# Performance work log

Hardware: AMD Instinct MI355X
Metric: run time of the kernel (lower is better)

Reference implementation:

```python
import jax, jax.numpy as jnp
import numpy as np

B, N, F_IN = 2048, 64, 49   # batch of molecules, max atoms, atom feature size
D, H, L = 256, 8, 6         # conv_dim, num_heads, n_GAT_layer
DK = D // H                 # per-head dim
FC = 128                    # fc_dim
ALPHA = 0.2                 # LeakyReLU slope in GAT
NEG_INF = -1e9


def setup_inputs() -> dict:
    key = jax.random.key(0)
    ks = jax.random.split(key, 10)
    # --- padded molecular graphs ---
    n_atoms = jax.random.randint(ks[0], (B,), 16, N + 1)
    valid = jnp.arange(N)[None, :] < n_atoms[:, None]                  # [B,N]
    r = jax.random.uniform(ks[1], (B, N, N))
    adj = ((r + jnp.swapaxes(r, 1, 2)) * 0.5) < 0.08                   # symmetric sparse bonds
    adj = adj | jnp.eye(N, dtype=bool)[None]                           # self loops
    adj = adj & valid[:, :, None] & valid[:, None, :]                  # zero padded atoms
    A = adj.astype(jnp.float32)                                        # [B,N,N]
    x = jax.random.normal(ks[2], (B, N, F_IN), dtype=jnp.float32)      # [B,N,49]
    # --- parameters (xavier-like scaling) ---
    W_emb = jax.random.normal(ks[3], (D, F_IN), dtype=jnp.float32) * 0.08
    gat_W = jax.random.normal(ks[4], (L, D, D), dtype=jnp.float32) * 0.06
    gat_b = jnp.zeros((L, D), dtype=jnp.float32)
    gat_a = jax.random.normal(ks[5], (L, H, 2 * DK), dtype=jnp.float32) * 0.1
    fc_W1 = jax.random.normal(ks[6], (FC, D), dtype=jnp.float32) * 0.07
    fc_b1 = jnp.zeros((FC,), dtype=jnp.float32)
    fc_W2 = jax.random.normal(ks[7], (FC, FC), dtype=jnp.float32) * 0.09
    fc_b2 = jnp.zeros((FC,), dtype=jnp.float32)
    fc_W3 = jax.random.normal(ks[8], (1, FC), dtype=jnp.float32) * 0.09
    fc_b3 = jnp.zeros((1,), dtype=jnp.float32)
    return dict(x=x, A=A, W_emb=W_emb, gat_W=gat_W, gat_b=gat_b, gat_a=gat_a,
                fc_W1=fc_W1, fc_b1=fc_b1, fc_W2=fc_W2, fc_b2=fc_b2,
                fc_W3=fc_W3, fc_b3=fc_b3)


def _gat_layer(x, A, W, b, a):
    # x: [B,N,D], A: [B,N,N], W: [D,D], b: [D], a: [H,2*DK]
    Bm, Nn, Dd = x.shape
    h = (x @ W.T + b).reshape(Bm, Nn, H, DK)                           # [B,N,H,DK]
    a_src, a_dst = a[:, :DK], a[:, DK:]                                # [H,DK]
    e_src = jnp.einsum('bnhd,hd->bnh', h, a_src)                       # [B,N,H]
    e_dst = jnp.einsum('bnhd,hd->bnh', h, a_dst)
    e = jax.nn.leaky_relu(e_src[:, :, None, :] + e_dst[:, None, :, :], ALPHA)  # [B,Ni,Nj,H]
    e = jnp.where((A > 0)[..., None], e, NEG_INF)                      # adjacency mask
    attn = jax.nn.softmax(e, axis=2)                                   # softmax over neighbors j
    out = jnp.einsum('bijh,bjhd->bihd', attn, h).reshape(Bm, Nn, Dd)
    return jax.nn.elu(out + x)                                         # residual + ELU


def reference(x, A, W_emb, gat_W, gat_b, gat_a,
              fc_W1, fc_b1, fc_W2, fc_b2, fc_W3, fc_b3):
    h = x @ W_emb.T                                                    # embedding (no bias)
    for l in range(L):                                                 # dropout p=0 -> identity
        h = _gat_layer(h, A, gat_W[l], gat_b[l], gat_a[l])
    # masked mean readout
    node_mask = (A.sum(-1) > 0).astype(h.dtype)                        # [B,N]
    w = node_mask / node_mask.sum(-1, keepdims=True)
    g = (h * w[..., None]).sum(1)                                      # [B,D]
    # dense head: 256 -> 128 -> 128 -> 1
    z = jax.nn.relu(g @ fc_W1.T + fc_b1)
    z = jax.nn.relu(z @ fc_W2.T + fc_b2)
    z = z @ fc_W3.T + fc_b3                                            # [B,1]
    return jax.nn.elu(z).squeeze(-1) + 1.5                             # [B]
```

## Files before the change

### kernel.cpp

```cpp
#include <hip/hip_runtime.h>
#include <cstdint>
#include <cstddef>

#define B_GRAPHS 2048
#define N_NODES  64
#define FIN      49
#define D_DIM    256
#define H_HEADS  8
#define DK_DIM   32
#define L_LAYERS 6
#define ALPHA    0.2f
#define LOG2E    1.4426950408889634f

#define M_FULL     (B_GRAPHS * N_NODES)
#define WSLAB      (256 * 256)

typedef __bf16 bf16x8 __attribute__((ext_vector_type(8)));
typedef __bf16 bf16x4 __attribute__((ext_vector_type(4)));
typedef float  f32x4  __attribute__((ext_vector_type(4)));

#define MFMA16(a, b, c) __builtin_amdgcn_mfma_f32_16x16x32_bf16(a, b, c, 0, 0, 0)

__device__ __forceinline__ float leaky(float t) { return t > 0.f ? t : ALPHA * t; }

#define LDS_H     0
#define LDS_V     32768
#define LDS_EI    49152
#define LDS_A     54272
#define LDS_BIAS  66560
#define LDS_BA    72704
#define LDS_AM    73088
#define LDS_VALID 73600
#define LDS_TOTAL 73632

__global__ void convert_weights(const float* __restrict__ W_emb,
                                const float* __restrict__ gat_W,
                                const float* __restrict__ gat_a,
                                const float* __restrict__ gat_b,
                                __bf16* __restrict__ Wemb_b,
                                __bf16* __restrict__ Wb,
                                float* __restrict__ ba)
{
    int idx = blockIdx.x * 256 + threadIdx.x;
    if (idx < 256 * 64) {
        int n = idx >> 6, k = idx & 63;
        float f = (k < FIN) ? W_emb[n * FIN + k] : 0.f;
        Wemb_b[idx] = (__bf16)f;
    }
    if (idx < L_LAYERS * 65536) {
        Wb[idx] = (__bf16)gat_W[idx];
    }
    int o2 = idx - L_LAYERS * 65536;
    if (o2 >= 0 && o2 < L_LAYERS * 16) {
        int l = o2 >> 4, c = o2 & 15;
        int hh = c >> 1, sd = c & 1;
        const float* av = gat_a + l * 512 + hh * 64 + sd * 32;
        const float* bp = gat_b + l * 256 + hh * 32;
        float s = 0.f;
        for (int d = 0; d < 32; d++) s += av[d] * bp[d];
        ba[o2] = s;
    }
}

__global__ void convert_x(const float* __restrict__ x, __bf16* __restrict__ xb)
{
    int idx = blockIdx.x * 256 + threadIdx.x;
    int m = idx >> 6, k = idx & 63;
    xb[idx] = (__bf16)((k < FIN) ? x[m * FIN + k] : 0.f);
}

__global__ __launch_bounds__(256, 2)
void mega_gat(const float* __restrict__ A,
              const __bf16* __restrict__ xb,
              const __bf16* __restrict__ Wemb,
              const __bf16* __restrict__ Wb_all,
              const float* __restrict__ gat_b_all,
              const float* __restrict__ a_all,
              const float* __restrict__ ba_all,
              const float* __restrict__ W1, const float* __restrict__ b1,
              const float* __restrict__ W2, const float* __restrict__ b2,
              const float* __restrict__ W3, const float* __restrict__ b3,
              float* __restrict__ out)
{
    __shared__ __align__(16) char smem[LDS_TOTAL];

    const int tid  = threadIdx.x;
    const int lane = tid & 63;
    const int w    = tid >> 6;
    const int q    = lane >> 4;
    const int d15  = lane & 15;
    const int g    = blockIdx.x;

    char*  vwbase   = smem + LDS_V + w * 4096;
    float* E        = (float*)(smem + LDS_EI + w * 1280);
    float* invv     = (float*)(smem + LDS_EI + w * 1280 + 1024);
    float* a_lds    = (float*)(smem + LDS_A);
    float* bias_lds = (float*)(smem + LDS_BIAS);
    float* ba_lds   = (float*)(smem + LDS_BA);
    unsigned long long* Am = (unsigned long long*)(smem + LDS_AM);

    auto h_off = [&](int i, int d) -> int {
        return i * 512 + ((((d >> 3) ^ (i & 7)) << 4)) + ((d & 7) << 1);
    };

    {
        const char* src = (const char*)(xb + (size_t)g * 4096);
        bf16x8 t0 = *(const bf16x8*)(src + tid * 16);
        bf16x8 t1 = *(const bf16x8*)(src + 4096 + tid * 16);
        int u0 = tid, u1 = 256 + tid;
        int r0 = u0 >> 3, s0 = u0 & 7;
        int r1 = u1 >> 3, s1 = u1 & 7;
        *(bf16x8*)(smem + LDS_V + r0 * 128 + ((s0 ^ (r0 & 7)) << 4)) = t0;
        *(bf16x8*)(smem + LDS_V + r1 * 128 + ((s1 ^ (r1 & 7)) << 4)) = t1;
    }
#pragma unroll
    for (int i = 0; i < 12; i++) a_lds[i * 256 + tid] = a_all[i * 256 + tid];
#pragma unroll
    for (int i = 0; i < 6; i++) bias_lds[i * 256 + tid] = gat_b_all[i * 256 + tid];
    if (tid < 96) ba_lds[tid] = ba_all[tid];
    {
        const float* Ab = A + (size_t)g * 4096;
#pragma unroll
        for (int rr = 0; rr < 16; rr++) {
            int r = w * 16 + rr;
            unsigned long long m = __ballot(Ab[r * 64 + lane] > 0.f);
            if (lane == 0) Am[r] = m;
        }
    }
    __syncthreads();

    if (w == 0) {
        unsigned long long rowm = Am[lane];
        unsigned long long vm = __ballot((rowm >> lane) & 1ULL);
        if (lane == 0) {
            *(unsigned long long*)(smem + LDS_VALID) = vm;
            *(float*)(smem + LDS_VALID + 8) = 1.f / (float)__popcll(vm);
        }
    }

    {
        f32x4 acc[4][4];
#pragma unroll
        for (int i = 0; i < 4; i++)
#pragma unroll
            for (int j = 0; j < 4; j++) acc[i][j] = (f32x4){0.f, 0.f, 0.f, 0.f};
#pragma unroll
        for (int ks = 0; ks < 2; ks++) {
            const int k0 = ks * 32 + q * 8;
            const int sl = ks * 4 + q;
            bf16x8 ah[4];
#pragma unroll
            for (int mf = 0; mf < 4; mf++) {
                int r = mf * 16 + d15;
                ah[mf] = *(const bf16x8*)(smem + LDS_V + r * 128 + ((sl ^ (r & 7)) << 4));
            }
#pragma unroll
            for (int nf = 0; nf < 4; nf++) {
                bf16x8 bh = *(const bf16x8*)(Wemb + (size_t)(w * 64 + nf * 16 + d15) * 64 + k0);
#pragma unroll
                for (int mf = 0; mf < 4; mf++)
                    acc[mf][nf] = MFMA16(ah[mf], bh, acc[mf][nf]);
            }
        }
#pragma unroll
        for (int nf = 0; nf < 4; nf++) {
            int d = w * 64 + nf * 16 + d15;
#pragma unroll
            for (int mf = 0; mf < 4; mf++)
#pragma unroll
                for (int rr = 0; rr < 4; rr++) {
                    int i = mf * 16 + q * 4 + rr;
                    *(__bf16*)(smem + h_off(i, d)) = (__bf16)acc[mf][nf][rr];
                }
        }
    }
    __syncthreads();

#pragma unroll 1
    for (int l = 0; l < L_LAYERS; l++) {
        const __bf16* Wl = Wb_all + (size_t)l * WSLAB;

        f32x4 acc[4][4];
#pragma unroll
        for (int i = 0; i < 4; i++)
#pragma unroll
            for (int j = 0; j < 4; j++) acc[i][j] = (f32x4){0.f, 0.f, 0.f, 0.f};

        bf16x8 breg[3][4];
        auto loadB = [&](int buf, int ks) {
            const int k0 = ks * 32 + q * 8;
#pragma unroll
            for (int nf = 0; nf < 4; nf++)
                breg[buf][nf] = *(const bf16x8*)(Wl + (size_t)(w * 64 + nf * 16 + d15) * 256 + k0);
        };
        loadB(0, 0);
        loadB(1, 1);

#pragma unroll
        for (int ks = 0; ks < 8; ks++) {
            if (ks + 2 < 8) loadB((ks + 2) % 3, ks + 2);
            bf16x8 ah[4];
            const int sl = ks * 4 + q;
#pragma unroll
            for (int mf = 0; mf < 4; mf++) {
                int r = mf * 16 + d15;
                ah[mf] = *(const bf16x8*)(smem + r * 512 + ((sl ^ (r & 7)) << 4));
            }
#pragma unroll
            for (int nf = 0; nf < 4; nf++)
#pragma unroll
                for (int mf = 0; mf < 4; mf++)
                    acc[mf][nf] = MFMA16(ah[mf], breg[ks % 3][nf], acc[mf][nf]);
        }

        __syncthreads();

        unsigned long long msk[4];
#pragma unroll
        for (int mf = 0; mf < 4; mf++) msk[mf] = Am[mf * 16 + d15];

#pragma unroll
        for (int hl = 0; hl < 2; hl++) {
            const int head = 2 * w + hl;

#pragma unroll
            for (int sd = 0; sd < 2; sd++) {
                float a0 = a_lds[l * 512 + head * 64 + sd * 32 + d15];
                float a1 = a_lds[l * 512 + head * 64 + sd * 32 + 16 + d15];
                float tmp[4][4];
#pragma unroll
                for (int mf = 0; mf < 4; mf++)
#pragma unroll
                    for (int rr = 0; rr < 4; rr++)
                        tmp[mf][rr] = acc[mf][2 * hl][rr] * a0 + acc[mf][2 * hl + 1][rr] * a1;
#pragma unroll
                for (int off = 1; off <= 8; off <<= 1)
#pragma unroll
                    for (int mf = 0; mf < 4; mf++)
#pragma unroll
                        for (int rr = 0; rr < 4; rr++)
                            tmp[mf][rr] += __shfl_xor(tmp[mf][rr], off);
                float bac = ba_lds[l * 16 + 2 * head + sd];
                if (d15 == 0) {
#pragma unroll
                    for (int mf = 0; mf < 4; mf++)
#pragma unroll
                        for (int rr = 0; rr < 4; rr++)
                            E[(hl * 2 + sd) * 64 + mf * 16 + q * 4 + rr] =
                                (tmp[mf][rr] + bac) * LOG2E;
                }
            }

#pragma unroll
            for (int nfl = 0; nfl < 2; nfl++) {
                const int nf = hl * 2 + nfl;
                const int d  = nfl * 16 + d15;
                const float bv = bias_lds[l * 256 + w * 64 + nf * 16 + d15];
                char* vb = vwbase + d * 128;
#pragma unroll
                for (int mf = 0; mf < 4; mf++) {
                    int s   = mf * 2 + (q >> 1);
                    int off = ((s ^ (d & 7)) << 4) + (q & 1) * 8;
                    bf16x4 h4;
#pragma unroll
                    for (int rr = 0; rr < 4; rr++)
                        h4[rr] = (__bf16)(acc[mf][nf][rr] + bv);
                    *(bf16x4*)(vb + off) = h4;
                }
            }

            float ev = E[(hl * 2 + 1) * 64 + lane];
#pragma unroll
            for (int off = 32; off; off >>= 1) ev = fmaxf(ev, __shfl_xor(ev, off));

            float esi[4], mh[4];
#pragma unroll
            for (int mf = 0; mf < 4; mf++) {
                esi[mf] = E[(hl * 2) * 64 + mf * 16 + d15];
                mh[mf]  = leaky(esi[mf] + ev);
            }

            f32x4 pv[4][2];
#pragma unroll
            for (int mf = 0; mf < 4; mf++) {
                pv[mf][0] = (f32x4){0.f, 0.f, 0.f, 0.f};
                pv[mf][1] = (f32x4){0.f, 0.f, 0.f, 0.f};
            }
            float rs[4] = {0.f, 0.f, 0.f, 0.f};

#pragma unroll
            for (int ksj = 0; ksj < 2; ksj++) {
                const int j8 = ksj * 32 + q * 8;
                const int s  = ksj * 4 + q;
                bf16x8 vh[2];
#pragma unroll
                for (int nf2 = 0; nf2 < 2; nf2++) {
                    int d = nf2 * 16 + d15;
                    vh[nf2] = *(const bf16x8*)(vwbase + d * 128 + ((s ^ (d & 7)) << 4));
                }
                float edv[8];
#pragma unroll
                for (int e = 0; e < 8; e++) edv[e] = E[(hl * 2 + 1) * 64 + j8 + e];

#pragma unroll
                for (int mf = 0; mf < 4; mf++) {
                    unsigned int mb = (unsigned int)(msk[mf] >> j8) & 0xffu;
                    bf16x8 ph;
                    float rsum = 0.f;
#pragma unroll
                    for (int e = 0; e < 8; e++) {
                        float t = leaky(esi[mf] + edv[e]);
                        float p = ((mb >> e) & 1u)
                                    ? __builtin_amdgcn_exp2f(t - mh[mf]) : 0.f;
                        rsum += p;
                        ph[e] = (__bf16)p;
                    }
                    rs[mf] += rsum;
#pragma unroll
                    for (int nf2 = 0; nf2 < 2; nf2++)
                        pv[mf][nf2] = MFMA16(ph, vh[nf2], pv[mf][nf2]);
                }
            }

#pragma unroll
            for (int mf = 0; mf < 4; mf++) {
                float r = rs[mf];
                r += __shfl_xor(r, 16);
                r += __shfl_xor(r, 32);
                if (q == 0) invv[mf * 16 + d15] = (r > 0.f) ? 1.f / r : 0.f;
            }

#pragma unroll
            for (int mf = 0; mf < 4; mf++) {
#pragma unroll
                for (int nf2 = 0; nf2 < 2; nf2++) {
                    int d = head * 32 + nf2 * 16 + d15;
#pragma unroll
                    for (int rr = 0; rr < 4; rr++) {
                        int i = mf * 16 + q * 4 + rr;
                        float inv = invv[i];
                        int hoff = h_off(i, d);
                        float old = (float)*(const __bf16*)(smem + hoff);
                        float o = pv[mf][nf2][rr] * inv + old;
                        o = o > 0.f ? o : __expf(o) - 1.f;
                        *(__bf16*)(smem + hoff) = (__bf16)o;
                    }
                }
            }
        }
        __syncthreads();
    }

    {
        unsigned long long vm = *(const unsigned long long*)(smem + LDS_VALID);
        float invc = *(const float*)(smem + LDS_VALID + 8);
        float gsum = 0.f;
#pragma unroll 8
        for (int n = 0; n < 64; n++)
            if ((vm >> n) & 1ULL)
                gsum += (float)*(const __bf16*)(smem + h_off(n, tid));

        float* gl = (float*)(smem + LDS_V);
        float* z1 = (float*)(smem + LDS_V + 1024);
        float* z2 = (float*)(smem + LDS_V + 1536);
        gl[tid] = gsum * invc;
        __syncthreads();

        if (tid < 128) {
            const float* wr = W1 + tid * 256;
            float z = 0.f;
#pragma unroll 8
            for (int k = 0; k < 256; k += 4) {
                float4 wv = *(const float4*)&wr[k];
                z += wv.x * gl[k] + wv.y * gl[k + 1] + wv.z * gl[k + 2] + wv.w * gl[k + 3];
            }
            z += b1[tid];
            z1[tid] = z > 0.f ? z : 0.f;
        }
        __syncthreads();

        if (tid < 128) {
            const float* wr = W2 + tid * 128;
            float z = 0.f;
#pragma unroll 8
            for (int k = 0; k < 128; k += 4) {
                float4 wv = *(const float4*)&wr[k];
                z += wv.x * z1[k] + wv.y * z1[k + 1] + wv.z * z1[k + 2] + wv.w * z1[k + 3];
            }
            z += b2[tid];
            z2[tid] = z > 0.f ? z : 0.f;
        }
        __syncthreads();

        if (tid < 64) {
            float p = W3[tid] * z2[tid] + W3[tid + 64] * z2[tid + 64];
#pragma unroll
            for (int off = 32; off; off >>= 1) p += __shfl_down(p, off);
            if (tid == 0) {
                float z = p + b3[0];
                out[g] = (z > 0.f ? z : __expf(z) - 1.f) + 1.5f;
            }
        }
    }
}

extern "C" void kernel_launch(void* const* d_in, const int* in_sizes, int n_in,
                              void* d_out, int out_size, void* d_ws, size_t ws_size,
                              hipStream_t stream)
{
    const float* x      = (const float*)d_in[0];
    const float* A      = (const float*)d_in[1];
    const float* W_emb  = (const float*)d_in[2];
    const float* gat_W  = (const float*)d_in[3];
    const float* gat_b  = (const float*)d_in[4];
    const float* gat_a  = (const float*)d_in[5];
    const float* fc_W1  = (const float*)d_in[6];
    const float* fc_b1  = (const float*)d_in[7];
    const float* fc_W2  = (const float*)d_in[8];
    const float* fc_b2  = (const float*)d_in[9];
    const float* fc_W3  = (const float*)d_in[10];
    const float* fc_b3  = (const float*)d_in[11];
    float* out = (float*)d_out;

    char* ws = (char*)d_ws;
    __bf16* xb     = (__bf16*)ws;
    __bf16* Wemb_b = (__bf16*)(ws + 16777216);
    __bf16* Wb     = (__bf16*)(ws + 16809984);
    float*  ba     = (float*)(ws + 17596416);

    int conv_total = L_LAYERS * 65536 + L_LAYERS * 16;
    convert_weights<<<(conv_total + 255) / 256, 256, 0, stream>>>(
        W_emb, gat_W, gat_a, gat_b, Wemb_b, Wb, ba);
    convert_x<<<M_FULL * 64 / 256, 256, 0, stream>>>(x, xb);

    mega_gat<<<B_GRAPHS, 256, 0, stream>>>(
        A, xb, Wemb_b, Wb, gat_b, gat_a, ba,
        fc_W1, fc_b1, fc_W2, fc_b2, fc_W3, fc_b3, out);
}
```

Before: 569.6 us.

## Skip GEMM and attention tiles for padded atoms using valid-node count

Reads the valid-node mask once, counts the valid atoms, and derives how many 16-row M tiles and 32-column neighbor K slabs actually contain valid atoms. The per-layer projection MFMAs, score reductions, softmax/PV MFMAs and residual-ELU writeback are then skipped for tiles made only of padding, and the softmax max ignores invalid lanes. It also raises wave priority around the MFMA block. This assumes valid atoms form a contiguous prefix, and rows in padded tiles keep stale values, which only the masked readout tolerates.

```diff
diff --git a/kernel.cpp b/kernel.cpp
--- a/kernel.cpp
+++ b/kernel.cpp
@@ -131,10 +131,10 @@
 
     if (w == 0) {
         unsigned long long rowm = Am[lane];
-        unsigned long long vm = __ballot((rowm >> lane) & 1ULL);
+        unsigned long long vmw = __ballot((rowm >> lane) & 1ULL);
         if (lane == 0) {
-            *(unsigned long long*)(smem + LDS_VALID) = vm;
-            *(float*)(smem + LDS_VALID + 8) = 1.f / (float)__popcll(vm);
+            *(unsigned long long*)(smem + LDS_VALID) = vmw;
+            *(float*)(smem + LDS_VALID + 8) = 1.f / (float)__popcll(vmw);
         }
     }
 
@@ -175,6 +175,12 @@
         }
     }
     __syncthreads();
+
+    const unsigned long long vm = *(const unsigned long long*)(smem + LDS_VALID);
+    const int nv   = __popcll(vm);
+    const int MFV  = (nv + 15) >> 4;
+    const int KSJV = (nv + 31) >> 5;
+    const bool lane_valid = (vm >> lane) & 1ULL;
 
 #pragma unroll 1
     for (int l = 0; l < L_LAYERS; l++) {
@@ -203,14 +209,19 @@
             const int sl = ks * 4 + q;
 #pragma unroll
             for (int mf = 0; mf < 4; mf++) {
-                int r = mf * 16 + d15;
-                ah[mf] = *(const bf16x8*)(smem + r * 512 + ((sl ^ (r & 7)) << 4));
-            }
+                if (mf < MFV) {
+                    int r = mf * 16 + d15;
+                    ah[mf] = *(const bf16x8*)(smem + r * 512 + ((sl ^ (r & 7)) << 4));
+                }
+            }
+            __builtin_amdgcn_s_setprio(1);
 #pragma unroll
             for (int nf = 0; nf < 4; nf++)
 #pragma unroll
                 for (int mf = 0; mf < 4; mf++)
-                    acc[mf][nf] = MFMA16(ah[mf], breg[ks % 3][nf], acc[mf][nf]);
+                    if (mf < MFV)
+                        acc[mf][nf] = MFMA16(ah[mf], breg[ks % 3][nf], acc[mf][nf]);
+            __builtin_amdgcn_s_setprio(0);
         }
 
         __syncthreads();
@@ -229,25 +240,30 @@
                 float a1 = a_lds[l * 512 + head * 64 + sd * 32 + 16 + d15];
                 float tmp[4][4];
 #pragma unroll
-                for (int mf = 0; mf < 4; mf++)
-#pragma unroll
-                    for (int rr = 0; rr < 4; rr++)
-                        tmp[mf][rr] = acc[mf][2 * hl][rr] * a0 + acc[mf][2 * hl + 1][rr] * a1;
+                for (int mf = 0; mf < 4; mf++) {
+                    if (mf < MFV) {
+#pragma unroll
+                        for (int rr = 0; rr < 4; rr++)
+                            tmp[mf][rr] = acc[mf][2 * hl][rr] * a0 + acc[mf][2 * hl + 1][rr] * a1;
+                    }
+                }
 #pragma unroll
                 for (int off = 1; off <= 8; off <<= 1)
 #pragma unroll
                     for (int mf = 0; mf < 4; mf++)
-#pragma unroll
-                        for (int rr = 0; rr < 4; rr++)
-                            tmp[mf][rr] += __shfl_xor(tmp[mf][rr], off);
+                        if (mf < MFV)
+#pragma unroll
+                            for (int rr = 0; rr < 4; rr++)
+                                tmp[mf][rr] += __shfl_xor(tmp[mf][rr], off);
                 float bac = ba_lds[l * 16 + 2 * head + sd];
                 if (d15 == 0) {
 #pragma unroll
                     for (int mf = 0; mf < 4; mf++)
-#pragma unroll
-                        for (int rr = 0; rr < 4; rr++)
-                            E[(hl * 2 + sd) * 64 + mf * 16 + q * 4 + rr] =
-                                (tmp[mf][rr] + bac) * LOG2E;
+                        if (mf < MFV)
+#pragma unroll
+                            for (int rr = 0; rr < 4; rr++)
+                                E[(hl * 2 + sd) * 64 + mf * 16 + q * 4 + rr] =
+                                    (tmp[mf][rr] + bac) * LOG2E;
                 }
             }
 
@@ -269,15 +285,17 @@
                 }
             }
 
-            float ev = E[(hl * 2 + 1) * 64 + lane];
+            float ev = lane_valid ? E[(hl * 2 + 1) * 64 + lane] : -1e30f;
 #pragma unroll
             for (int off = 32; off; off >>= 1) ev = fmaxf(ev, __shfl_xor(ev, off));
 
             float esi[4], mh[4];
 #pragma unroll
             for (int mf = 0; mf < 4; mf++) {
-                esi[mf] = E[(hl * 2) * 64 + mf * 16 + d15];
-                mh[mf]  = leaky(esi[mf] + ev);
+                if (mf < MFV) {
+                    esi[mf] = E[(hl * 2) * 64 + mf * 16 + d15];
+                    mh[mf]  = leaky(esi[mf] + ev);
+                }
             }
 
             f32x4 pv[4][2];
@@ -290,69 +308,76 @@
 
 #pragma unroll
             for (int ksj = 0; ksj < 2; ksj++) {
-                const int j8 = ksj * 32 + q * 8;
-                const int s  = ksj * 4 + q;
-                bf16x8 vh[2];
-#pragma unroll
-                for (int nf2 = 0; nf2 < 2; nf2++) {
-                    int d = nf2 * 16 + d15;
-                    vh[nf2] = *(const bf16x8*)(vwbase + d * 128 + ((s ^ (d & 7)) << 4));
-                }
-                float edv[8];
-#pragma unroll
-                for (int e = 0; e < 8; e++) edv[e] = E[(hl * 2 + 1) * 64 + j8 + e];
-
-#pragma unroll
-                for (int mf = 0; mf < 4; mf++) {
-                    unsigned int mb = (unsigned int)(msk[mf] >> j8) & 0xffu;
-                    bf16x8 ph;
-                    float rsum = 0.f;
-#pragma unroll
-                    for (int e = 0; e < 8; e++) {
-                        float t = leaky(esi[mf] + edv[e]);
-                        float p = ((mb >> e) & 1u)
-                                    ? __builtin_amdgcn_exp2f(t - mh[mf]) : 0.f;
-                        rsum += p;
-                        ph[e] = (__bf16)p;
+                if (ksj < KSJV) {
+                    const int j8 = ksj * 32 + q * 8;
+                    const int s  = ksj * 4 + q;
+                    bf16x8 vh[2];
+#pragma unroll
+                    for (int nf2 = 0; nf2 < 2; nf2++) {
+                        int d = nf2 * 16 + d15;
+                        vh[nf2] = *(const bf16x8*)(vwbase + d * 128 + ((s ^ (d & 7)) << 4));
                     }
-                    rs[mf] += rsum;
-#pragma unroll
-                    for (int nf2 = 0; nf2 < 2; nf2++)
-                        pv[mf][nf2] = MFMA16(ph, vh[nf2], pv[mf][nf2]);
-                }
-            }
-
-#pragma unroll
-            for (int mf = 0; mf < 4; mf++) {
-                float r = rs[mf];
-                r += __shfl_xor(r, 16);
-                r += __shfl_xor(r, 32);
-                if (q == 0) invv[mf * 16 + d15] = (r > 0.f) ? 1.f / r : 0.f;
-            }
-
-#pragma unroll
-            for (int mf = 0; mf < 4; mf++) {
-#pragma unroll
-                for (int nf2 = 0; nf2 < 2; nf2++) {
-                    int d = head * 32 + nf2 * 16 + d15;
-#pragma unroll
-                    for (int rr = 0; rr < 4; rr++) {
-                        int i = mf * 16 + q * 4 + rr;
-                        float inv = invv[i];
-                        int hoff = h_off(i, d);
-                        float old = (float)*(const __bf16*)(smem + hoff);
-                        float o = pv[mf][nf2][rr] * inv + old;
-                        o = o > 0.f ? o : __expf(o) - 1.f;
-                        *(__bf16*)(smem + hoff) = (__bf16)o;
+                    float edv[8];
+#pragma unroll
+                    for (int e = 0; e < 8; e++) edv[e] = E[(hl * 2 + 1) * 64 + j8 + e];
+
+#pragma unroll
+                    for (int mf = 0; mf < 4; mf++) {
+                        if (mf < MFV) {
+                            unsigned int mb = (unsigned int)(msk[mf] >> j8) & 0xffu;
+                            bf16x8 ph;
+                            float rsum = 0.f;
+#pragma unroll
+                            for (int e = 0; e < 8; e++) {
+                                float t = leaky(esi[mf] + edv[e]);
+                                float p = ((mb >> e) & 1u)
+                                            ? __builtin_amdgcn_exp2f(t - mh[mf]) : 0.f;
+                                rsum += p;
+                                ph[e] = (__bf16)p;
+                            }
+                            rs[mf] += rsum;
+#pragma unroll
+                            for (int nf2 = 0; nf2 < 2; nf2++)
+                                pv[mf][nf2] = MFMA16(ph, vh[nf2], pv[mf][nf2]);
+                        }
                     }
                 }
             }
+
+#pragma unroll
+            for (int mf = 0; mf < 4; mf++) {
+                if (mf < MFV) {
+                    float r = rs[mf];
+                    r += __shfl_xor(r, 16);
+                    r += __shfl_xor(r, 32);
+                    if (q == 0) invv[mf * 16 + d15] = (r > 0.f) ? 1.f / r : 0.f;
+                }
+            }
+
+#pragma unroll
+            for (int mf = 0; mf < 4; mf++) {
+                if (mf < MFV) {
+#pragma unroll
+                    for (int nf2 = 0; nf2 < 2; nf2++) {
+                        int d = head * 32 + nf2 * 16 + d15;
+#pragma unroll
+                        for (int rr = 0; rr < 4; rr++) {
+                            int i = mf * 16 + q * 4 + rr;
+                            float inv = invv[i];
+                            int hoff = h_off(i, d);
+                            float old = (float)*(const __bf16*)(smem + hoff);
+                            float o = pv[mf][nf2][rr] * inv + old;
+                            o = o > 0.f ? o : __expf(o) - 1.f;
+                            *(__bf16*)(smem + hoff) = (__bf16)o;
+                        }
+                    }
+                }
+            }
         }
         __syncthreads();
     }
 
     {
-        unsigned long long vm = *(const unsigned long long*)(smem + LDS_VALID);
         float invc = *(const float*)(smem + LDS_VALID + 8);
         float gsum = 0.f;
 #pragma unroll 8
```

Measured after the change: 606.4 us. 6.5% more time.

## Shrink LDS footprint to fit three blocks per CU

Applied to the files above, without the earlier changes.

Removes the LDS staging of attention vectors, biases and bias-attention sums; each layer now loads its per-lane values from global memory into registers. The inverse row-sum buffer reuses the slot of the source-score row in the E scratch, so LDS drops from about 72KB to about 53KB. Launch bounds are raised to 3 blocks per CU to gain occupancy. The cost is more register pressure under a tighter VGPR budget, which could cause spills, plus small per-layer global loads.

```diff
diff --git a/kernel.cpp b/kernel.cpp
--- a/kernel.cpp
+++ b/kernel.cpp
@@ -25,13 +25,10 @@
 
 #define LDS_H     0
 #define LDS_V     32768
-#define LDS_EI    49152
-#define LDS_A     54272
-#define LDS_BIAS  66560
-#define LDS_BA    72704
-#define LDS_AM    73088
-#define LDS_VALID 73600
-#define LDS_TOTAL 73632
+#define LDS_E     49152
+#define LDS_AM    53248
+#define LDS_VALID 53760
+#define LDS_TOTAL 53776
 
 __global__ void convert_weights(const float* __restrict__ W_emb,
                                 const float* __restrict__ gat_W,
@@ -69,7 +66,7 @@
     xb[idx] = (__bf16)((k < FIN) ? x[m * FIN + k] : 0.f);
 }
 
-__global__ __launch_bounds__(256, 2)
+__global__ __launch_bounds__(256, 3)
 void mega_gat(const float* __restrict__ A,
               const __bf16* __restrict__ xb,
               const __bf16* __restrict__ Wemb,
@@ -91,12 +88,8 @@
     const int d15  = lane & 15;
     const int g    = blockIdx.x;
 
-    char*  vwbase   = smem + LDS_V + w * 4096;
-    float* E        = (float*)(smem + LDS_EI + w * 1280);
-    float* invv     = (float*)(smem + LDS_EI + w * 1280 + 1024);
-    float* a_lds    = (float*)(smem + LDS_A);
-    float* bias_lds = (float*)(smem + LDS_BIAS);
-    float* ba_lds   = (float*)(smem + LDS_BA);
+    char*  vwbase = smem + LDS_V + w * 4096;
+    float* E      = (float*)(smem + LDS_E + w * 1024);
     unsigned long long* Am = (unsigned long long*)(smem + LDS_AM);
 
     auto h_off = [&](int i, int d) -> int {
@@ -113,11 +106,6 @@
         *(bf16x8*)(smem + LDS_V + r0 * 128 + ((s0 ^ (r0 & 7)) << 4)) = t0;
         *(bf16x8*)(smem + LDS_V + r1 * 128 + ((s1 ^ (r1 & 7)) << 4)) = t1;
     }
-#pragma unroll
-    for (int i = 0; i < 12; i++) a_lds[i * 256 + tid] = a_all[i * 256 + tid];
-#pragma unroll
-    for (int i = 0; i < 6; i++) bias_lds[i * 256 + tid] = gat_b_all[i * 256 + tid];
-    if (tid < 96) ba_lds[tid] = ba_all[tid];
     {
         const float* Ab = A + (size_t)g * 4096;
 #pragma unroll
@@ -131,10 +119,10 @@
 
     if (w == 0) {
         unsigned long long rowm = Am[lane];
-        unsigned long long vm = __ballot((rowm >> lane) & 1ULL);
+        unsigned long long vmw = __ballot((rowm >> lane) & 1ULL);
         if (lane == 0) {
-            *(unsigned long long*)(smem + LDS_VALID) = vm;
-            *(float*)(smem + LDS_VALID + 8) = 1.f / (float)__popcll(vm);
+            *(unsigned long long*)(smem + LDS_VALID) = vmw;
+            *(float*)(smem + LDS_VALID + 8) = 1.f / (float)__popcll(vmw);
         }
     }
 
@@ -176,9 +164,26 @@
     }
     __syncthreads();
 
+    const unsigned long long vm = *(const unsigned long long*)(smem + LDS_VALID);
+
 #pragma unroll 1
     for (int l = 0; l < L_LAYERS; l++) {
         const __bf16* Wl = Wb_all + (size_t)l * WSLAB;
+
+        float a0r[2][2], a1r[2][2], bar[2][2], bvreg[4];
+#pragma unroll
+        for (int hp = 0; hp < 2; hp++) {
+            const int head = 2 * w + hp;
+#pragma unroll
+            for (int sd = 0; sd < 2; sd++) {
+                a0r[hp][sd] = a_all[l * 512 + head * 64 + sd * 32 + d15];
+                a1r[hp][sd] = a_all[l * 512 + head * 64 + sd * 32 + 16 + d15];
+                bar[hp][sd] = ba_all[l * 16 + 2 * head + sd];
+            }
+        }
+#pragma unroll
+        for (int nf = 0; nf < 4; nf++)
+            bvreg[nf] = gat_b_all[l * 256 + w * 64 + nf * 16 + d15];
 
         f32x4 acc[4][4];
 #pragma unroll
@@ -225,8 +230,8 @@
 
 #pragma unroll
             for (int sd = 0; sd < 2; sd++) {
-                float a0 = a_lds[l * 512 + head * 64 + sd * 32 + d15];
-                float a1 = a_lds[l * 512 + head * 64 + sd * 32 + 16 + d15];
+                float a0 = a0r[hl][sd];
+                float a1 = a1r[hl][sd];
                 float tmp[4][4];
 #pragma unroll
                 for (int mf = 0; mf < 4; mf++)
@@ -240,7 +245,7 @@
 #pragma unroll
                         for (int rr = 0; rr < 4; rr++)
                             tmp[mf][rr] += __shfl_xor(tmp[mf][rr], off);
-                float bac = ba_lds[l * 16 + 2 * head + sd];
+                float bac = bar[hl][sd];
                 if (d15 == 0) {
 #pragma unroll
                     for (int mf = 0; mf < 4; mf++)
@@ -255,7 +260,7 @@
             for (int nfl = 0; nfl < 2; nfl++) {
                 const int nf = hl * 2 + nfl;
                 const int d  = nfl * 16 + d15;
-                const float bv = bias_lds[l * 256 + w * 64 + nf * 16 + d15];
+                const float bv = bvreg[nf];
                 char* vb = vwbase + d * 128;
 #pragma unroll
                 for (int mf = 0; mf < 4; mf++) {
@@ -327,7 +332,8 @@
                 float r = rs[mf];
                 r += __shfl_xor(r, 16);
                 r += __shfl_xor(r, 32);
-                if (q == 0) invv[mf * 16 + d15] = (r > 0.f) ? 1.f / r : 0.f;
+                if (q == 0)
+                    E[(hl * 2) * 64 + mf * 16 + d15] = (r > 0.f) ? 1.f / r : 0.f;
             }
 
 #pragma unroll
@@ -338,7 +344,7 @@
 #pragma unroll
                     for (int rr = 0; rr < 4; rr++) {
                         int i = mf * 16 + q * 4 + rr;
-                        float inv = invv[i];
+                        float inv = E[(hl * 2) * 64 + i];
                         int hoff = h_off(i, d);
                         float old = (float)*(const __bf16*)(smem + hoff);
                         float o = pv[mf][nf2][rr] * inv + old;
@@ -352,7 +358,6 @@
     }
 
     {
-        unsigned long long vm = *(const unsigned long long*)(smem + LDS_VALID);
         float invc = *(const float*)(smem + LDS_VALID + 8);
         float gsum = 0.f;
 #pragma unroll 8
```

Measured after the change: 1.109 ms. 94.7% more time.
